# Kernel tuning notes

Measured on AMD Instinct MI355X. Metric: run time of the kernel, lower is better.

## Reference

```python
import jax, jax.numpy as jnp
import numpy as np


def setup_inputs() -> dict:
    key = jax.random.key(0)
    k_v, k_w, k_b, k_c = jax.random.split(key, 4)
    B, V, H = 32768, 1024, 128
    # Binary visible input, as RBM_BB (Bernoulli-Bernoulli) expects
    v_0 = (jax.random.uniform(k_v, (B, V, 1)) < 0.5).astype(jnp.float32)
    W = 0.01 * jax.random.normal(k_w, (H, V), dtype=jnp.float32)
    b = 0.01 * jax.random.normal(k_b, (V, 1), dtype=jnp.float32)
    c = 0.01 * jax.random.normal(k_c, (H, 1), dtype=jnp.float32)
    return {"v_0": v_0, "W": W, "b": b, "c": c, "num_sampling_iter": 4}


def reference(v_0, W, b, c, num_sampling_iter):
    """Block Gibbs sampling for a Bernoulli-Bernoulli RBM.

    v: [B, V, 1], h: [B, H, 1]; W: [H, V], b: [V, 1], c: [H, 1].
    Returns (v_given_h, h_given_v, h_given_v_0), all detached samples.
    """
    dtype = v_0.dtype
    key = jax.random.key(42)

    def p_h_given_v(v):  # [B,V,1] -> [B,H,1]
        return jax.nn.sigmoid(jnp.matmul(W, v) + c)

    def p_v_given_h(h):  # [B,H,1] -> [B,V,1]
        return jax.nn.sigmoid(jnp.matmul(W.T, h) + b)

    def bernoulli(k, p):
        # sample is detached (torch .detach()) -> stop_gradient
        return jax.lax.stop_gradient(jax.random.bernoulli(k, p).astype(dtype))

    keys = jax.random.split(key, num_sampling_iter + 1)
    h_given_v_0 = bernoulli(keys[0], p_h_given_v(v_0))

    def gibbs_step(h, k):
        k_v, k_h = jax.random.split(k)
        v = bernoulli(k_v, p_v_given_h(h))
        h_new = bernoulli(k_h, p_h_given_v(v))
        return h_new, v

    h_given_v, vs = jax.lax.scan(gibbs_step, h_given_v_0, keys[1:])
    v_given_h = vs[-1]
    return (v_given_h, h_given_v, h_given_v_0)
```

## Files before the change

kernel.cpp:

```cpp
#include <hip/hip_runtime.h>
#include <cstdint>


#define TF_ROT(x, r) (((x) << (r)) | ((x) >> (32 - (r))))

__host__ __device__ __forceinline__ void threefry2x32(
    uint32_t k0, uint32_t k1, uint32_t x0, uint32_t x1,
    uint32_t &o0, uint32_t &o1) {
  const uint32_t ks2 = k0 ^ k1 ^ 0x1BD11BDAu;
  x0 += k0; x1 += k1;
#define TF_R(r) { x0 += x1; x1 = TF_ROT(x1, r); x1 ^= x0; }
  TF_R(13) TF_R(15) TF_R(26) TF_R(6)
  x0 += k1; x1 += ks2 + 1u;
  TF_R(17) TF_R(29) TF_R(16) TF_R(24)
  x0 += ks2; x1 += k0 + 2u;
  TF_R(13) TF_R(15) TF_R(26) TF_R(6)
  x0 += k0; x1 += k1 + 3u;
  TF_R(17) TF_R(29) TF_R(16) TF_R(24)
  x0 += k1; x1 += ks2 + 4u;
  TF_R(13) TF_R(15) TF_R(26) TF_R(6)
  x0 += ks2; x1 += k0 + 5u;
#undef TF_R
  o0 = x0; o1 = x1;
}

__device__ __forceinline__ float cephes_expf(float xin) {
  float xc = fminf(xin, 88.3762626647950f);
  xc = fmaxf(xc, -88.3762626647949f);
  float fx = floorf(xc * 1.44269504088896341f + 0.5f);
  float tmp = 0.693359375f * fx;
  float z2  = -2.12194440e-4f * fx;
  float x = xc - tmp;
  x = x - z2;
  float z = x * x;
  float y = 1.9875691500E-4f * x + 1.3981999507E-3f;
  y = y * x + 8.3334519073E-3f;
  y = y * x + 4.1665795894E-2f;
  y = y * x + 1.6666665459E-1f;
  y = y * x + 5.0000001201E-1f;
  y = y * z + x;
  y = 1.0f + y;
  int n = (int)fx;
  float p2n = __uint_as_float((uint32_t)(n + 127) << 23);
  return fmaxf(y * p2n, xin);
}

__device__ __forceinline__ void sample_store(
    float tot, const float* bias, float* out,
    long b, int ng, int N_total, uint32_t k0, uint32_t k1) {
  float pre = tot + bias[ng];
  float p   = 1.0f / (1.0f + cephes_expf(-pre));
  uint32_t flat = (uint32_t)(b * N_total + ng);
  uint32_t w0, w1;
  threefry2x32(k0, k1, 0u, flat, w0, w1);
  uint32_t bits = w0 ^ w1;
  float u = __uint_as_float((bits >> 9) | 0x3f800000u) - 1.0f;
  out[(long)b * N_total + ng] = (u < p) ? 1.0f : 0.0f;
}

template <bool SAMPLE, bool SINGLE_PANEL>
__global__ __launch_bounds__(256) void gemm_tile(
    const float* __restrict__ A,
    const float* __restrict__ Bt,
    const float* __restrict__ bias,
    float* __restrict__ out,
    int ldA, int N_total, int K, int tiles_per_panel, int Mtot,
    uint32_t k0, uint32_t k1)
{
  __shared__ float As[64 * 32];
  __shared__ float Bs[128 * 32];
  const int t  = threadIdx.x;
  const int tx = t & 15;
  const int ty = t >> 4;
  const int bm = blockIdx.x;
  const int j0 = blockIdx.y << 7;

  int kb, ke;
  float* outp = out;
  if (SAMPLE) { kb = 0; ke = K; }
  else {
    const int z = blockIdx.z;
    kb = z * 320;
    ke = min(K, kb + 320);
    outp = out + (size_t)z * Mtot * 128;
  }

  float cur[4][8];
  float tot[4][8];
#pragma unroll
  for (int i = 0; i < 4; ++i)
#pragma unroll
    for (int j = 0; j < 8; ++j) { cur[i][j] = 0.0f; if (!SINGLE_PANEL) tot[i][j] = 0.0f; }

  const long arow = (long)bm * 64 * ldA;
  const int t0 = kb >> 5, t1 = ke >> 5;

  for (int tki = t0; tki < t1; ++tki) {
    const int kc = tki << 5;
#pragma unroll
    for (int r = 0; r < 2; ++r) {
      int q = t + 256 * r;
      int m = q >> 3;
      int c = q & 7;
      float4 val = *(const float4*)(A + arow + (long)m * ldA + kc + 4 * c);
      *(float4*)(As + m * 32 + ((c ^ (m & 7)) << 2)) = val;
    }
#pragma unroll
    for (int r = 0; r < 4; ++r) {
      int q = t + 256 * r;
      int n = q >> 3;
      int c = q & 7;
      float4 val = *(const float4*)(Bt + (long)(j0 + n) * ldA + kc + 4 * c);
      *(float4*)(Bs + n * 32 + ((c ^ (n & 7)) << 2)) = val;
    }
    __syncthreads();

#pragma unroll
    for (int c = 0; c < 8; ++c) {
      float4 av[4], bv[8];
#pragma unroll
      for (int i = 0; i < 4; ++i) {
        int m = ty + 16 * i;
        av[i] = *(const float4*)(As + m * 32 + ((c ^ (m & 7)) << 2));
      }
#pragma unroll
      for (int j = 0; j < 8; ++j) {
        int n = tx + 16 * j;
        bv[j] = *(const float4*)(Bs + n * 32 + ((c ^ (n & 7)) << 2));
      }
#pragma unroll
      for (int i = 0; i < 4; ++i)
#pragma unroll
        for (int j = 0; j < 8; ++j) {
          cur[i][j] = __fmaf_rn(av[i].x, bv[j].x, cur[i][j]);
          cur[i][j] = __fmaf_rn(av[i].y, bv[j].y, cur[i][j]);
          cur[i][j] = __fmaf_rn(av[i].z, bv[j].z, cur[i][j]);
          cur[i][j] = __fmaf_rn(av[i].w, bv[j].w, cur[i][j]);
        }
    }
    __syncthreads();

    if (!SINGLE_PANEL) {
      if (((tki - t0 + 1) % tiles_per_panel == 0) || (tki == t1 - 1)) {
#pragma unroll
        for (int i = 0; i < 4; ++i)
#pragma unroll
          for (int j = 0; j < 8; ++j) { tot[i][j] += cur[i][j]; cur[i][j] = 0.0f; }
      }
    }
  }

#pragma unroll
  for (int i = 0; i < 4; ++i) {
    const int m = ty + 16 * i;
    const long b = (long)bm * 64 + m;
#pragma unroll
    for (int j = 0; j < 8; ++j) {
      const int n  = tx + 16 * j;
      const int ng = j0 + n;
      const float v = SINGLE_PANEL ? cur[i][j] : tot[i][j];
      if (SAMPLE) {
        sample_store(v, bias, outp, b, ng, N_total, k0, k1);
      } else {
        outp[b * 128 + ng] = v;
      }
    }
  }
}

__global__ __launch_bounds__(256) void combine_sample(
    const float* __restrict__ partials,
    const float* __restrict__ bias,
    float* __restrict__ out,
    int Mtot, uint32_t k0, uint32_t k1)
{
  const long idx = (long)blockIdx.x * 256 + threadIdx.x;
  const long S = (long)Mtot * 128;
  float p0 = partials[idx];
  float p1 = partials[S + idx];
  float p2 = partials[2 * S + idx];
  float p3 = partials[3 * S + idx];
  float tot = ((p0 + p1) + p2) + p3;
  float pre = tot + bias[(int)(idx & 127)];
  float p   = 1.0f / (1.0f + cephes_expf(-pre));
  uint32_t w0, w1;
  threefry2x32(k0, k1, 0u, (uint32_t)idx, w0, w1);
  uint32_t bits = w0 ^ w1;
  float u = __uint_as_float((bits >> 9) | 0x3f800000u) - 1.0f;
  out[idx] = (u < p) ? 1.0f : 0.0f;
}

__global__ void transpose_W(const float* __restrict__ W, float* __restrict__ Wt) {
  __shared__ float tile[32][33];
  int bx = blockIdx.x, by = blockIdx.y;
  int x = threadIdx.x, y = threadIdx.y;
  tile[y][x] = W[(by * 32 + y) * 1024 + bx * 32 + x];
  __syncthreads();
  Wt[(bx * 32 + y) * 128 + by * 32 + x] = tile[x][y];
}

extern "C" void kernel_launch(void* const* d_in, const int* in_sizes, int n_in,
                              void* d_out, int out_size, void* d_ws, size_t ws_size,
                              hipStream_t stream) {
  const float* v0 = (const float*)d_in[0];
  const float* W  = (const float*)d_in[1];
  const float* bb = (const float*)d_in[2];
  const float* cb = (const float*)d_in[3];
  const int B = in_sizes[0] / 1024;

  float* out    = (float*)d_out;
  float* out_v  = out;
  float* out_h1 = out + (size_t)B * 1024;
  float* out_h2 = out_h1 + (size_t)B * 128;

  float* Wt       = (float*)d_ws;
  float* h_ws     = Wt + 1024 * 128;
  float* partials = h_ws + (size_t)B * 128;
  const size_t need = (size_t)(1024 * 128 + (size_t)B * 128 * 5) * 4;
  const bool use_split = ws_size >= need;

  uint32_t kt[5][2], kv[5][2], kh[5][2];
  for (uint32_t i = 0; i < 5; ++i) threefry2x32(0u, 42u, 0u, i, kt[i][0], kt[i][1]);
  for (int t = 1; t <= 4; ++t) {
    threefry2x32(kt[t][0], kt[t][1], 0u, 0u, kv[t][0], kv[t][1]);
    threefry2x32(kt[t][0], kt[t][1], 0u, 1u, kh[t][0], kh[t][1]);
  }

  transpose_W<<<dim3(32, 4), dim3(32, 32), 0, stream>>>(W, Wt);

  const int MB = B / 64;

  auto h_step = [&](const float* vin, float* hdst, uint32_t hk0, uint32_t hk1) {
    if (use_split) {
      gemm_tile<false, true><<<dim3(MB, 1, 4), 256, 0, stream>>>(
          vin, W, nullptr, partials, 1024, 128, 1024, 1000, B, 0u, 0u);
      combine_sample<<<dim3(B * 128 / 256), 256, 0, stream>>>(
          partials, cb, hdst, B, hk0, hk1);
    } else {
      gemm_tile<true, false><<<dim3(MB, 1, 1), 256, 0, stream>>>(
          vin, W, cb, hdst, 1024, 128, 1024, 10, B, hk0, hk1);
    }
  };

  h_step(v0, out_h2, kt[0][0], kt[0][1]);

  const float* h = out_h2;
  for (int t = 1; t <= 4; ++t) {
    gemm_tile<true, true><<<dim3(MB, 8, 1), 256, 0, stream>>>(
        h, Wt, bb, out_v, 128, 1024, 128, 10, B, kv[t][0], kv[t][1]);
    float* hdst = (t == 4) ? out_h1 : h_ws;
    h_step(out_v, hdst, kh[t][0], kh[t][1]);
    h = hdst;
  }
}
```

Measured before the change: 1.602 ms.

## Use packed FP32 FMA with k-major B tile and vectorized output stores

Rewrites the GEMM tile inner loop to use v_pk_fma_f32 inline asm on float2 accumulators, and stores the B tile transposed (k-major, padded stride) so each thread reads contiguous float4 columns. The A tile now uses a padded stride instead of an XOR swizzle. Output columns per thread become four contiguous values, allowing float4 stores for both sampled and partial outputs. It also adds a launch-bounds occupancy hint. The aim is to halve FMA instruction count and cut scattered stores, at the cost of scalar transposing LDS writes and more complex register usage.

```diff
diff --git a/kernel.cpp b/kernel.cpp
--- a/kernel.cpp
+++ b/kernel.cpp
@@ -45,21 +45,34 @@
   return fmaxf(y * p2n, xin);
 }
 
-__device__ __forceinline__ void sample_store(
-    float tot, const float* bias, float* out,
-    long b, int ng, int N_total, uint32_t k0, uint32_t k1) {
-  float pre = tot + bias[ng];
+__device__ __forceinline__ float sample_val(
+    float tot, float bias, long b, int ng, int N_total,
+    uint32_t k0, uint32_t k1) {
+  float pre = tot + bias;
   float p   = 1.0f / (1.0f + cephes_expf(-pre));
   uint32_t flat = (uint32_t)(b * N_total + ng);
   uint32_t w0, w1;
   threefry2x32(k0, k1, 0u, flat, w0, w1);
   uint32_t bits = w0 ^ w1;
   float u = __uint_as_float((bits >> 9) | 0x3f800000u) - 1.0f;
-  out[(long)b * N_total + ng] = (u < p) ? 1.0f : 0.0f;
-}
+  return (u < p) ? 1.0f : 0.0f;
+}
+
+typedef float float2v __attribute__((ext_vector_type(2)));
+typedef float float4v __attribute__((ext_vector_type(4)));
+
+#define PKFMA_W0(acc, apair, b2) \
+  asm("v_pk_fma_f32 %0, %1, %2, %0 op_sel:[0,0,0] op_sel_hi:[0,1,1]" \
+      : "+v"(acc) : "v"(apair), "v"(b2))
+#define PKFMA_W1(acc, apair, b2) \
+  asm("v_pk_fma_f32 %0, %1, %2, %0 op_sel:[1,0,0] op_sel_hi:[1,1,1]" \
+      : "+v"(acc) : "v"(apair), "v"(b2))
+
+#define ASTRIDE 36
+#define BSTRIDE 130
 
 template <bool SAMPLE, bool SINGLE_PANEL>
-__global__ __launch_bounds__(256) void gemm_tile(
+__global__ __launch_bounds__(256, 4) void gemm_tile(
     const float* __restrict__ A,
     const float* __restrict__ Bt,
     const float* __restrict__ bias,
@@ -67,8 +80,8 @@
     int ldA, int N_total, int K, int tiles_per_panel, int Mtot,
     uint32_t k0, uint32_t k1)
 {
-  __shared__ float As[64 * 32];
-  __shared__ float Bs[128 * 32];
+  __shared__ float As[64 * ASTRIDE];
+  __shared__ float Bs[32 * BSTRIDE];
   const int t  = threadIdx.x;
   const int tx = t & 15;
   const int ty = t >> 4;
@@ -85,15 +98,21 @@
     outp = out + (size_t)z * Mtot * 128;
   }
 
-  float cur[4][8];
-  float tot[4][8];
+  float2v cur[4][4];
+  float2v tot[4][4];
 #pragma unroll
   for (int i = 0; i < 4; ++i)
 #pragma unroll
-    for (int j = 0; j < 8; ++j) { cur[i][j] = 0.0f; if (!SINGLE_PANEL) tot[i][j] = 0.0f; }
+    for (int p = 0; p < 4; ++p) {
+      cur[i][p] = (float2v)(0.0f);
+      if (!SINGLE_PANEL) tot[i][p] = (float2v)(0.0f);
+    }
 
   const long arow = (long)bm * 64 * ldA;
   const int t0 = kb >> 5, t1 = ke >> 5;
+
+  const float* aP = As + ty * ASTRIDE;
+  const float* bP = Bs + 4 * tx;
 
   for (int tki = t0; tki < t1; ++tki) {
     const int kc = tki << 5;
@@ -103,7 +122,7 @@
       int m = q >> 3;
       int c = q & 7;
       float4 val = *(const float4*)(A + arow + (long)m * ldA + kc + 4 * c);
-      *(float4*)(As + m * 32 + ((c ^ (m & 7)) << 2)) = val;
+      *(float4*)(As + m * ASTRIDE + 4 * c) = val;
     }
 #pragma unroll
     for (int r = 0; r < 4; ++r) {
@@ -111,32 +130,48 @@
       int n = q >> 3;
       int c = q & 7;
       float4 val = *(const float4*)(Bt + (long)(j0 + n) * ldA + kc + 4 * c);
-      *(float4*)(Bs + n * 32 + ((c ^ (n & 7)) << 2)) = val;
+      float* w = Bs + (4 * c) * BSTRIDE + n;
+      w[0]           = val.x;
+      w[BSTRIDE]     = val.y;
+      w[2 * BSTRIDE] = val.z;
+      w[3 * BSTRIDE] = val.w;
     }
     __syncthreads();
 
 #pragma unroll
     for (int c = 0; c < 8; ++c) {
-      float4 av[4], bv[8];
+      float2v alo[4], ahi[4];
 #pragma unroll
       for (int i = 0; i < 4; ++i) {
-        int m = ty + 16 * i;
-        av[i] = *(const float4*)(As + m * 32 + ((c ^ (m & 7)) << 2));
+        float4v a4 = *(const float4v*)(aP + i * 16 * ASTRIDE + 4 * c);
+        alo[i] = __builtin_shufflevector(a4, a4, 0, 1);
+        ahi[i] = __builtin_shufflevector(a4, a4, 2, 3);
       }
 #pragma unroll
-      for (int j = 0; j < 8; ++j) {
-        int n = tx + 16 * j;
-        bv[j] = *(const float4*)(Bs + n * 32 + ((c ^ (n & 7)) << 2));
+      for (int cc = 0; cc < 4; ++cc) {
+        const float* brow = bP + (4 * c + cc) * BSTRIDE;
+        float4v b0 = *(const float4v*)(brow);
+        float4v b1 = *(const float4v*)(brow + 64);
+        float2v b00 = __builtin_shufflevector(b0, b0, 0, 1);
+        float2v b01 = __builtin_shufflevector(b0, b0, 2, 3);
+        float2v b10 = __builtin_shufflevector(b1, b1, 0, 1);
+        float2v b11 = __builtin_shufflevector(b1, b1, 2, 3);
+#pragma unroll
+        for (int i = 0; i < 4; ++i) {
+          float2v ap = (cc < 2) ? alo[i] : ahi[i];
+          if ((cc & 1) == 0) {
+            PKFMA_W0(cur[i][0], ap, b00);
+            PKFMA_W0(cur[i][1], ap, b01);
+            PKFMA_W0(cur[i][2], ap, b10);
+            PKFMA_W0(cur[i][3], ap, b11);
+          } else {
+            PKFMA_W1(cur[i][0], ap, b00);
+            PKFMA_W1(cur[i][1], ap, b01);
+            PKFMA_W1(cur[i][2], ap, b10);
+            PKFMA_W1(cur[i][3], ap, b11);
+          }
+        }
       }
-#pragma unroll
-      for (int i = 0; i < 4; ++i)
-#pragma unroll
-        for (int j = 0; j < 8; ++j) {
-          cur[i][j] = __fmaf_rn(av[i].x, bv[j].x, cur[i][j]);
-          cur[i][j] = __fmaf_rn(av[i].y, bv[j].y, cur[i][j]);
-          cur[i][j] = __fmaf_rn(av[i].z, bv[j].z, cur[i][j]);
-          cur[i][j] = __fmaf_rn(av[i].w, bv[j].w, cur[i][j]);
-        }
     }
     __syncthreads();
 
@@ -145,7 +180,10 @@
 #pragma unroll
         for (int i = 0; i < 4; ++i)
 #pragma unroll
-          for (int j = 0; j < 8; ++j) { tot[i][j] += cur[i][j]; cur[i][j] = 0.0f; }
+          for (int p = 0; p < 4; ++p) {
+            tot[i][p] += cur[i][p];
+            cur[i][p] = (float2v)(0.0f);
+          }
       }
     }
   }
@@ -155,14 +193,21 @@
     const int m = ty + 16 * i;
     const long b = (long)bm * 64 + m;
 #pragma unroll
-    for (int j = 0; j < 8; ++j) {
-      const int n  = tx + 16 * j;
-      const int ng = j0 + n;
-      const float v = SINGLE_PANEL ? cur[i][j] : tot[i][j];
+    for (int jq = 0; jq < 2; ++jq) {
+      const int n0 = 4 * tx + 64 * jq;
+      float2v pA = SINGLE_PANEL ? cur[i][2 * jq]     : tot[i][2 * jq];
+      float2v pB = SINGLE_PANEL ? cur[i][2 * jq + 1] : tot[i][2 * jq + 1];
+      float4 o;
       if (SAMPLE) {
-        sample_store(v, bias, outp, b, ng, N_total, k0, k1);
+        const int ng = j0 + n0;
+        o.x = sample_val(pA.x, bias[ng],     b, ng,     N_total, k0, k1);
+        o.y = sample_val(pA.y, bias[ng + 1], b, ng + 1, N_total, k0, k1);
+        o.z = sample_val(pB.x, bias[ng + 2], b, ng + 2, N_total, k0, k1);
+        o.w = sample_val(pB.y, bias[ng + 3], b, ng + 3, N_total, k0, k1);
+        *(float4*)(outp + b * N_total + ng) = o;
       } else {
-        outp[b * 128 + ng] = v;
+        o.x = pA.x; o.y = pA.y; o.z = pB.x; o.w = pB.y;
+        *(float4*)(outp + b * 128 + n0) = o;
       }
     }
   }
```

Result: slower. 2.958 ms (+84.6%).

## Load GEMM tiles via direct global-to-LDS and use k-major B layout

Applied to the files above, without the earlier changes.

The GEMM tile kernel now loads A and B tiles with the AMD global_load_lds builtin, so data goes straight into LDS without passing through registers. The B operand is read in k-major form, with the call sites swapping W and Wt. The inner loop becomes an outer-product update, where each thread reads float4 rows of B and broadcasts scalar A values. Outputs are written as float4 vectors, the end-of-loop barrier is folded into a barrier at the start of each iteration, and launch bounds request 5 blocks per SIMD for occupancy. The XOR swizzle on the A tile is dropped, which risks LDS bank conflicts on A reads.

```diff
diff --git a/kernel.cpp b/kernel.cpp
--- a/kernel.cpp
+++ b/kernel.cpp
@@ -45,33 +45,40 @@
   return fmaxf(y * p2n, xin);
 }
 
-__device__ __forceinline__ void sample_store(
-    float tot, const float* bias, float* out,
-    long b, int ng, int N_total, uint32_t k0, uint32_t k1) {
-  float pre = tot + bias[ng];
+__device__ __forceinline__ float sample_val(
+    float tot, float bias, long b, int ng, int N_total,
+    uint32_t k0, uint32_t k1) {
+  float pre = tot + bias;
   float p   = 1.0f / (1.0f + cephes_expf(-pre));
   uint32_t flat = (uint32_t)(b * N_total + ng);
   uint32_t w0, w1;
   threefry2x32(k0, k1, 0u, flat, w0, w1);
   uint32_t bits = w0 ^ w1;
   float u = __uint_as_float((bits >> 9) | 0x3f800000u) - 1.0f;
-  out[(long)b * N_total + ng] = (u < p) ? 1.0f : 0.0f;
+  return (u < p) ? 1.0f : 0.0f;
+}
+
+__device__ __forceinline__ void gl2lds16(const float* g, float* l) {
+  __builtin_amdgcn_global_load_lds(
+      (const __attribute__((address_space(1))) void*)g,
+      (__attribute__((address_space(3))) void*)l, 16, 0, 0);
 }
 
 template <bool SAMPLE, bool SINGLE_PANEL>
-__global__ __launch_bounds__(256) void gemm_tile(
+__global__ __launch_bounds__(256, 5) void gemm_tile(
     const float* __restrict__ A,
-    const float* __restrict__ Bt,
+    const float* __restrict__ Bkm,
     const float* __restrict__ bias,
     float* __restrict__ out,
-    int ldA, int N_total, int K, int tiles_per_panel, int Mtot,
+    int lda, int ldb, int N_total, int K, int tiles_per_panel, int Mtot,
     uint32_t k0, uint32_t k1)
 {
   __shared__ float As[64 * 32];
-  __shared__ float Bs[128 * 32];
+  __shared__ float Bs[32 * 128];
   const int t  = threadIdx.x;
   const int tx = t & 15;
   const int ty = t >> 4;
+  const int w  = t >> 6;
   const int bm = blockIdx.x;
   const int j0 = blockIdx.y << 7;
 
@@ -92,53 +99,56 @@
 #pragma unroll
     for (int j = 0; j < 8; ++j) { cur[i][j] = 0.0f; if (!SINGLE_PANEL) tot[i][j] = 0.0f; }
 
-  const long arow = (long)bm * 64 * ldA;
+  const long arow = (long)bm * 64 * lda;
   const int t0 = kb >> 5, t1 = ke >> 5;
+
+  const float* aP = As + ty * 32;
+  const float* bP = Bs + 4 * tx;
 
   for (int tki = t0; tki < t1; ++tki) {
     const int kc = tki << 5;
+    __syncthreads();
 #pragma unroll
     for (int r = 0; r < 2; ++r) {
-      int q = t + 256 * r;
-      int m = q >> 3;
-      int c = q & 7;
-      float4 val = *(const float4*)(A + arow + (long)m * ldA + kc + 4 * c);
-      *(float4*)(As + m * 32 + ((c ^ (m & 7)) << 2)) = val;
+      int slot = r * 256 + t;
+      int m = slot >> 3, c = slot & 7;
+      gl2lds16(A + arow + (long)m * lda + kc + 4 * c,
+               As + (r * 256 + w * 64) * 4);
     }
 #pragma unroll
     for (int r = 0; r < 4; ++r) {
-      int q = t + 256 * r;
-      int n = q >> 3;
-      int c = q & 7;
-      float4 val = *(const float4*)(Bt + (long)(j0 + n) * ldA + kc + 4 * c);
-      *(float4*)(Bs + n * 32 + ((c ^ (n & 7)) << 2)) = val;
+      int slot = r * 256 + t;
+      int kk = slot >> 5, nc = slot & 31;
+      gl2lds16(Bkm + (long)(kc + kk) * ldb + j0 + 4 * nc,
+               Bs + (r * 256 + w * 64) * 4);
     }
     __syncthreads();
 
 #pragma unroll
     for (int c = 0; c < 8; ++c) {
-      float4 av[4], bv[8];
-#pragma unroll
-      for (int i = 0; i < 4; ++i) {
-        int m = ty + 16 * i;
-        av[i] = *(const float4*)(As + m * 32 + ((c ^ (m & 7)) << 2));
+      float4 av[4];
+#pragma unroll
+      for (int i = 0; i < 4; ++i)
+        av[i] = *(const float4*)(aP + i * 16 * 32 + 4 * c);
+#pragma unroll
+      for (int cc = 0; cc < 4; ++cc) {
+        const float* brow = bP + (4 * c + cc) * 128;
+        float4 b0 = *(const float4*)(brow);
+        float4 b1 = *(const float4*)(brow + 64);
+#pragma unroll
+        for (int i = 0; i < 4; ++i) {
+          const float a = ((const float*)&av[i])[cc];
+          cur[i][0] = __fmaf_rn(a, b0.x, cur[i][0]);
+          cur[i][1] = __fmaf_rn(a, b0.y, cur[i][1]);
+          cur[i][2] = __fmaf_rn(a, b0.z, cur[i][2]);
+          cur[i][3] = __fmaf_rn(a, b0.w, cur[i][3]);
+          cur[i][4] = __fmaf_rn(a, b1.x, cur[i][4]);
+          cur[i][5] = __fmaf_rn(a, b1.y, cur[i][5]);
+          cur[i][6] = __fmaf_rn(a, b1.z, cur[i][6]);
+          cur[i][7] = __fmaf_rn(a, b1.w, cur[i][7]);
+        }
       }
-#pragma unroll
-      for (int j = 0; j < 8; ++j) {
-        int n = tx + 16 * j;
-        bv[j] = *(const float4*)(Bs + n * 32 + ((c ^ (n & 7)) << 2));
-      }
-#pragma unroll
-      for (int i = 0; i < 4; ++i)
-#pragma unroll
-        for (int j = 0; j < 8; ++j) {
-          cur[i][j] = __fmaf_rn(av[i].x, bv[j].x, cur[i][j]);
-          cur[i][j] = __fmaf_rn(av[i].y, bv[j].y, cur[i][j]);
-          cur[i][j] = __fmaf_rn(av[i].z, bv[j].z, cur[i][j]);
-          cur[i][j] = __fmaf_rn(av[i].w, bv[j].w, cur[i][j]);
-        }
-    }
-    __syncthreads();
+    }
 
     if (!SINGLE_PANEL) {
       if (((tki - t0 + 1) % tiles_per_panel == 0) || (tki == t1 - 1)) {
@@ -155,14 +165,21 @@
     const int m = ty + 16 * i;
     const long b = (long)bm * 64 + m;
 #pragma unroll
-    for (int j = 0; j < 8; ++j) {
-      const int n  = tx + 16 * j;
-      const int ng = j0 + n;
-      const float v = SINGLE_PANEL ? cur[i][j] : tot[i][j];
+    for (int jq = 0; jq < 2; ++jq) {
+      const int n0 = 4 * tx + 64 * jq;
+      float4 o;
+      const float* acc = SINGLE_PANEL ? cur[i] : tot[i];
       if (SAMPLE) {
-        sample_store(v, bias, outp, b, ng, N_total, k0, k1);
+        const int ng = j0 + n0;
+        o.x = sample_val(acc[4 * jq + 0], bias[ng],     b, ng,     N_total, k0, k1);
+        o.y = sample_val(acc[4 * jq + 1], bias[ng + 1], b, ng + 1, N_total, k0, k1);
+        o.z = sample_val(acc[4 * jq + 2], bias[ng + 2], b, ng + 2, N_total, k0, k1);
+        o.w = sample_val(acc[4 * jq + 3], bias[ng + 3], b, ng + 3, N_total, k0, k1);
+        *(float4*)(outp + b * N_total + ng) = o;
       } else {
-        outp[b * 128 + ng] = v;
+        o.x = acc[4 * jq + 0]; o.y = acc[4 * jq + 1];
+        o.z = acc[4 * jq + 2]; o.w = acc[4 * jq + 3];
+        *(float4*)(outp + b * 128 + n0) = o;
       }
     }
   }
@@ -233,12 +250,12 @@
   auto h_step = [&](const float* vin, float* hdst, uint32_t hk0, uint32_t hk1) {
     if (use_split) {
       gemm_tile<false, true><<<dim3(MB, 1, 4), 256, 0, stream>>>(
-          vin, W, nullptr, partials, 1024, 128, 1024, 1000, B, 0u, 0u);
+          vin, Wt, nullptr, partials, 1024, 128, 128, 1024, 1000, B, 0u, 0u);
       combine_sample<<<dim3(B * 128 / 256), 256, 0, stream>>>(
           partials, cb, hdst, B, hk0, hk1);
     } else {
       gemm_tile<true, false><<<dim3(MB, 1, 1), 256, 0, stream>>>(
-          vin, W, cb, hdst, 1024, 128, 1024, 10, B, hk0, hk1);
+          vin, Wt, cb, hdst, 1024, 128, 128, 1024, 10, B, hk0, hk1);
     }
   };
 
@@ -247,7 +264,7 @@
   const float* h = out_h2;
   for (int t = 1; t <= 4; ++t) {
     gemm_tile<true, true><<<dim3(MB, 8, 1), 256, 0, stream>>>(
-        h, Wt, bb, out_v, 128, 1024, 128, 10, B, kv[t][0], kv[t][1]);
+        h, W, bb, out_v, 128, 1024, 1024, 128, 10, B, kv[t][0], kv[t][1]);
     float* hdst = (t == 4) ? out_h1 : h_ws;
     h_step(out_v, hdst, kh[t][0], kh[t][1]);
     h = hdst;
```

New measurement: 1.464 ms. -8.6%, faster.
